# Kernel tuning notes

Measured on AMD Instinct MI355X. Metric: run time of the kernel, lower is better.

## Reference

```python
import jax, jax.numpy as jnp
import numpy as np

B, N, E = 262144, 14, 12
THRESHOLD = 0.3


def setup_inputs() -> dict:
    key = jax.random.key(0)
    k1, k2 = jax.random.split(key)
    pos = jax.random.normal(k1, (B, N, 3), dtype=jnp.float32)
    rot = jax.random.normal(k2, (B, N, 9), dtype=jnp.float32)
    # two 7-node kinematic chains: left arm nodes 0..6, right arm nodes 7..13
    left = np.stack([np.arange(6), np.arange(1, 7)])
    right = np.stack([np.arange(7, 13), np.arange(8, 14)])
    edge_index = jnp.asarray(np.concatenate([left, right], axis=1), dtype=jnp.int32)  # [2, 12]
    ee_mask = jnp.zeros((N, 1), dtype=bool).at[6, 0].set(True).at[13, 0].set(True)
    return {"pos": pos, "rot": rot, "edge_index": edge_index, "ee_mask": ee_mask}


def _capsule_capsule_dist_square(p0, p1, q0, q1):
    # p*: [B, K, 3] left capsules (vary along axis j), q*: [B, K, 3] right capsules (vary along axis i)
    dp = p1 - p0                                  # [B, K, 3]
    dq = q1 - q0                                  # [B, K, 3]
    diff0 = p0[:, None, :, :] - q0[:, :, None, :]  # [B, K(i=q), K(j=p), 3]
    a = jnp.sum(dp * dp, -1)[:, None, :]          # [B, 1, K]
    c = jnp.sum(dq * dq, -1)[:, :, None]          # [B, K, 1]
    b = jnp.einsum('bjd,bid->bij', dp, dq)        # [B, K, K]
    d = jnp.sum(dp[:, None, :, :] * diff0, -1)
    e = jnp.sum(dq[:, :, None, :] * diff0, -1)
    det = a * c - b * b
    bte, ctd, ate, btd = b * e, c * d, a * e, b * d
    s = jnp.zeros_like(det)
    t = jnp.zeros_like(det)
    one = jnp.ones_like(det)
    s = jnp.where((det > 0) & (bte <= ctd) & (e <= 0) & (-d >= a), one, s)
    s = jnp.where((det > 0) & (bte <= ctd) & (e <= 0) & (-d < a) & (-d > 0), -d / a, s)
    t = jnp.where((det > 0) & (bte <= ctd) & (e > 0) & (e < c), e / c, t)
    s = jnp.where((det > 0) & (bte <= ctd) & (e > 0) & (e >= c) & (b - d >= a), one, s)
    s = jnp.where((det > 0) & (bte <= ctd) & (e > 0) & (e >= c) & (b - d < a) & (b - d > 0), (b - d) / a, s)
    t = jnp.where((det > 0) & (bte <= ctd) & (e > 0) & (e >= c), one, t)
    s = jnp.where((det > 0) & (bte > ctd) & (bte - ctd >= det) & (b + e <= 0) & (-d > 0) & (-d < a), -d / a, s)
    s = jnp.where((det > 0) & (bte > ctd) & (bte - ctd >= det) & (b + e <= 0) & (-d > 0) & (-d >= a), one, s)
    s = jnp.where((det > 0) & (bte > ctd) & (bte - ctd >= det) & (b + e > 0) & (b + e < c), one, s)
    t = jnp.where((det > 0) & (bte > ctd) & (bte - ctd >= det) & (b + e > 0) & (b + e < c), (b + e) / c, t)
    s = jnp.where((det > 0) & (bte > ctd) & (bte - ctd >= det) & (b + e > 0) & (b + e >= c) & (b - d > 0) & (b - d < a), (b - d) / a, s)
    s = jnp.where((det > 0) & (bte > ctd) & (bte - ctd >= det) & (b + e > 0) & (b + e >= c) & (b - d > 0) & (b - d >= a), one, s)
    t = jnp.where((det > 0) & (bte > ctd) & (bte - ctd >= det) & (b + e > 0) & (b + e >= c), one, t)
    s = jnp.where((det > 0) & (bte > ctd) & (bte - ctd < det) & (ate <= btd) & (-d > 0) & (-d >= a), one, s)
    s = jnp.where((det > 0) & (bte > ctd) & (bte - ctd < det) & (ate <= btd) & (-d > 0) & (-d < a), -d / a, s)
    s = jnp.where((det > 0) & (bte > ctd) & (bte - ctd < det) & (ate > btd) & (ate - btd >= det) & (b - d > 0) & (b - d >= a), one, s)
    s = jnp.where((det > 0) & (bte > ctd) & (bte - ctd < det) & (ate > btd) & (ate - btd >= det) & (b - d > 0) & (b - d < a), (b - d) / a, s)
    t = jnp.where((det > 0) & (bte > ctd) & (bte - ctd < det) & (ate > btd) & (ate - btd >= det), one, t)
    s = jnp.where((det > 0) & (bte > ctd) & (bte - ctd < det) & (ate > btd) & (ate - btd < det), (bte - ctd) / det, s)
    t = jnp.where((det > 0) & (bte > ctd) & (bte - ctd < det) & (ate > btd) & (ate - btd < det), (ate - btd) / det, t)
    s = jnp.where((det <= 0) & (e <= 0) & (-d > 0) & (-d >= a), one, s)
    s = jnp.where((det <= 0) & (e <= 0) & (-d > 0) & (-d < a), -d / a, s)
    s = jnp.where((det <= 0) & (e > 0) & (e >= c) & (b - d > 0) & (b - d >= a), one, s)
    s = jnp.where((det <= 0) & (e > 0) & (e >= c) & (b - d > 0) & (b - d < a), (b - d) / a, s)
    t = jnp.where((det <= 0) & (e > 0) & (e >= c), one, t)
    t = jnp.where((det <= 0) & (e > 0) & (e < c), e / c, t)
    # original code detaches s and t before forming w
    s = jax.lax.stop_gradient(s)
    t = jax.lax.stop_gradient(t)
    w = diff0 + s[..., None] * dp[:, None, :, :] - t[..., None] * dq[:, :, None, :]
    return jnp.sum(w * w, -1)  # [B, K, K]


def reference(pos, rot, edge_index, ee_mask):
    bsz, n_nodes = pos.shape[0], pos.shape[1]
    n_edges = edge_index.shape[1]
    half = n_edges // 2
    p0 = pos[:, edge_index[0]]  # [B, E, 3]
    p1 = pos[:, edge_index[1]]
    l_p0, r_p0 = p0[:, :half], p0[:, half:]
    l_p1, r_p1 = p1[:, :half], p1[:, half:]
    # exactly 2 end-effectors (left, right) marked in ee_mask
    ee_idx = jnp.nonzero(ee_mask[:, 0], size=2)[0]
    ee_pos = pos[:, ee_idx]                         # [B, 2, 3]  (left, right)
    ee_rot = rot[:, ee_idx].reshape(bsz, 2, 3, 3)   # [B, 2, 3, 3]
    offset = jnp.array([0.0, 0.0, 0.2], dtype=pos.dtype)
    hand_pos = jnp.einsum('beij,j->bei', ee_rot, offset) + ee_pos  # [B, 2, 3]
    l_p0 = jnp.concatenate([l_p0, ee_pos[:, 0:1]], axis=1)   # [B, E/2+1, 3]
    l_p1 = jnp.concatenate([l_p1, hand_pos[:, 0:1]], axis=1)
    r_p0 = jnp.concatenate([r_p0, ee_pos[:, 1:2]], axis=1)
    r_p1 = jnp.concatenate([r_p1, hand_pos[:, 1:2]], axis=1)
    dist_square = _capsule_capsule_dist_square(l_p0, l_p1, r_p0, r_p1)  # [B, 7, 7]
    mask = (dist_square < 0.1 ** 2) & (dist_square > 0)
    special = (dist_square[:, 6, 6] > THRESHOLD ** 2) & (dist_square[:, 6, 6] > 0)
    mask = mask.at[:, 6, 6].set(special)
    loss = jnp.sum(jnp.where(mask, jnp.exp(-dist_square), jnp.zeros_like(dist_square))) / bsz
    return loss
```

## Files before the change

### kernel.cpp

```cpp
#include <hip/hip_runtime.h>


__device__ __forceinline__ float rcpf(float x) { return __builtin_amdgcn_rcpf(x); }
__device__ __forceinline__ float clamp01(float x) {
    return __builtin_amdgcn_fmed3f(x, 0.0f, 1.0f);
}

__device__ __forceinline__ float cap_dist2(
    float px0, float py0, float pz0, float px1, float py1, float pz1,
    float qx0, float qy0, float qz0, float qx1, float qy1, float qz1)
{
    const float dpx = px1 - px0, dpy = py1 - py0, dpz = pz1 - pz0;
    const float dqx = qx1 - qx0, dqy = qy1 - qy0, dqz = qz1 - qz0;
    const float rx  = px0 - qx0, ry  = py0 - qy0, rz  = pz0 - qz0;

    const float a = dpx*dpx + dpy*dpy + dpz*dpz;
    const float c = dqx*dqx + dqy*dqy + dqz*dqz;
    const float b = dpx*dqx + dpy*dqy + dpz*dqz;
    const float d = dpx*rx + dpy*ry + dpz*rz;
    const float e = dqx*rx + dqy*ry + dqz*rz;
    const float det = a*c - b*b;

    const float rcp_a = rcpf(a);
    const float rcp_c = rcpf(c);

    const float f  = b*e - c*d;
    const float s0 = (det > 0.0f) ? clamp01(f * rcpf(det)) : 0.0f;

    const float tn = b*s0 + e;
    const float t  = clamp01(tn * rcp_c);

    const float sA = clamp01(-d * rcp_a);
    const float sB = clamp01((b - d) * rcp_a);
    const float s  = (tn < 0.0f) ? sA : ((tn > c) ? sB : s0);

    const float wx = rx + s*dpx - t*dqx;
    const float wy = ry + s*dpy - t*dqy;
    const float wz = rz + s*dpz - t*dqz;
    return wx*wx + wy*wy + wz*wz;
}

#define BT 128

__global__ __launch_bounds__(BT) void collision_loss_kernel(
    const float* __restrict__ pos,
    const float* __restrict__ rot,
    float* __restrict__ out)
{
    __shared__ float2 sbuf[BT * 21];
    __shared__ float wsum[2];

    const int tid       = threadIdx.x;
    const int blockBase = blockIdx.x * BT;
    const int b         = blockBase + tid;

    const float* rb = rot + (size_t)b * 126;
    const float r6x = rb[ 56], r6y = rb[ 59], r6z = rb[ 62];
    const float rdx = rb[119], rdy = rb[122], rdz = rb[125];

    const float2* g2 = reinterpret_cast<const float2*>(pos + (size_t)blockBase * 42);
    #pragma unroll
    for (int k = 0; k < 21; ++k) {
        const int idx = k * BT + tid;
        sbuf[idx] = g2[idx];
    }
    __syncthreads();

    const float2* m2 = sbuf + tid * 21;
    const float2 u0  = m2[0],  u1  = m2[1],  u2  = m2[2],  u3  = m2[3];
    const float2 u4  = m2[4],  u5  = m2[5],  u6  = m2[6],  u7  = m2[7];
    const float2 u8  = m2[8],  u9  = m2[9],  u10 = m2[10], u11 = m2[11];
    const float2 u12 = m2[12], u13 = m2[13], u14 = m2[14], u15 = m2[15];
    const float2 u16 = m2[16], u17 = m2[17], u18 = m2[18], u19 = m2[19];
    const float2 u20 = m2[20];

    const float n0x=u0.x,  n0y=u0.y,  n0z=u1.x;
    const float n1x=u1.y,  n1y=u2.x,  n1z=u2.y;
    const float n2x=u3.x,  n2y=u3.y,  n2z=u4.x;
    const float n3x=u4.y,  n3y=u5.x,  n3z=u5.y;
    const float n4x=u6.x,  n4y=u6.y,  n4z=u7.x;
    const float n5x=u7.y,  n5y=u8.x,  n5z=u8.y;
    const float n6x=u9.x,  n6y=u9.y,  n6z=u10.x;
    const float n7x=u10.y, n7y=u11.x, n7z=u11.y;
    const float n8x=u12.x, n8y=u12.y, n8z=u13.x;
    const float n9x=u13.y, n9y=u14.x, n9z=u14.y;
    const float n10x=u15.x, n10y=u15.y, n10z=u16.x;
    const float n11x=u16.y, n11y=u17.x, n11z=u17.y;
    const float n12x=u18.x, n12y=u18.y, n12z=u19.x;
    const float n13x=u19.y, n13y=u20.x, n13z=u20.y;

    const float hlx = n6x  + 0.2f * r6x;
    const float hly = n6y  + 0.2f * r6y;
    const float hlz = n6z  + 0.2f * r6z;
    const float hrx = n13x + 0.2f * rdx;
    const float hry = n13y + 0.2f * rdy;
    const float hrz = n13z + 0.2f * rdz;

    float sum = 0.0f;

    auto acc = [&](float p0x, float p0y, float p0z,
                   float p1x, float p1y, float p1z,
                   float q0x, float q0y, float q0z,
                   float q1x, float q1y, float q1z, bool special) {
        const float d2 = cap_dist2(p0x,p0y,p0z, p1x,p1y,p1z,
                                   q0x,q0y,q0z, q1x,q1y,q1z);
        const bool m = special ? (d2 > 0.09f)
                               : ((d2 < 0.01f) && (d2 > 0.0f));
        sum += m ? __expf(-d2) : 0.0f;
    };

    #define LROW(QX0,QY0,QZ0,QX1,QY1,QZ1,SP)                                  \
        acc(n0x,n0y,n0z, n1x,n1y,n1z, QX0,QY0,QZ0, QX1,QY1,QZ1, false);       \
        acc(n1x,n1y,n1z, n2x,n2y,n2z, QX0,QY0,QZ0, QX1,QY1,QZ1, false);       \
        acc(n2x,n2y,n2z, n3x,n3y,n3z, QX0,QY0,QZ0, QX1,QY1,QZ1, false);       \
        acc(n3x,n3y,n3z, n4x,n4y,n4z, QX0,QY0,QZ0, QX1,QY1,QZ1, false);       \
        acc(n4x,n4y,n4z, n5x,n5y,n5z, QX0,QY0,QZ0, QX1,QY1,QZ1, false);       \
        acc(n5x,n5y,n5z, n6x,n6y,n6z, QX0,QY0,QZ0, QX1,QY1,QZ1, false);       \
        acc(n6x,n6y,n6z, hlx,hly,hlz, QX0,QY0,QZ0, QX1,QY1,QZ1, SP);

    LROW(n7x, n7y, n7z,  n8x, n8y, n8z,  false)
    LROW(n8x, n8y, n8z,  n9x, n9y, n9z,  false)
    LROW(n9x, n9y, n9z,  n10x,n10y,n10z, false)
    LROW(n10x,n10y,n10z, n11x,n11y,n11z, false)
    LROW(n11x,n11y,n11z, n12x,n12y,n12z, false)
    LROW(n12x,n12y,n12z, n13x,n13y,n13z, false)
    LROW(n13x,n13y,n13z, hrx, hry, hrz,  true)
    #undef LROW

    #pragma unroll
    for (int off = 32; off > 0; off >>= 1)
        sum += __shfl_down(sum, off, 64);
    const int wave = tid >> 6;
    if ((tid & 63) == 0) wsum[wave] = sum;
    __syncthreads();
    if (tid == 0) {
        atomicAdd(out, (wsum[0] + wsum[1]) * (1.0f / 262144.0f));
    }
}

extern "C" void kernel_launch(void* const* d_in, const int* in_sizes, int n_in,
                              void* d_out, int out_size, void* d_ws, size_t ws_size,
                              hipStream_t stream) {
    const float* pos = (const float*)d_in[0];
    const float* rot = (const float*)d_in[1];
    float* out = (float*)d_out;

    const int B = in_sizes[0] / 42;
    hipMemsetAsync(out, 0, sizeof(float), stream);

    collision_loss_kernel<<<B / BT, BT, 0, stream>>>(pos, rot, out);
}
```

Baseline: 218.4 us.

## Process two batch tiles per block with register prefetch and per-wave LDS slabs

```diff
diff --git a/kernel.cpp b/kernel.cpp
--- a/kernel.cpp
+++ b/kernel.cpp
@@ -41,32 +41,13 @@
 }
 
 #define BT 128
+#define PB 2
 
-__global__ __launch_bounds__(BT) void collision_loss_kernel(
-    const float* __restrict__ pos,
-    const float* __restrict__ rot,
-    float* __restrict__ out)
+__device__ __forceinline__ float phase_compute(
+    const float2* __restrict__ m2,
+    float r6x, float r6y, float r6z,
+    float rdx, float rdy, float rdz)
 {
-    __shared__ float2 sbuf[BT * 21];
-    __shared__ float wsum[2];
-
-    const int tid       = threadIdx.x;
-    const int blockBase = blockIdx.x * BT;
-    const int b         = blockBase + tid;
-
-    const float* rb = rot + (size_t)b * 126;
-    const float r6x = rb[ 56], r6y = rb[ 59], r6z = rb[ 62];
-    const float rdx = rb[119], rdy = rb[122], rdz = rb[125];
-
-    const float2* g2 = reinterpret_cast<const float2*>(pos + (size_t)blockBase * 42);
-    #pragma unroll
-    for (int k = 0; k < 21; ++k) {
-        const int idx = k * BT + tid;
-        sbuf[idx] = g2[idx];
-    }
-    __syncthreads();
-
-    const float2* m2 = sbuf + tid * 21;
     const float2 u0  = m2[0],  u1  = m2[1],  u2  = m2[2],  u3  = m2[3];
     const float2 u4  = m2[4],  u5  = m2[5],  u6  = m2[6],  u7  = m2[7];
     const float2 u8  = m2[8],  u9  = m2[9],  u10 = m2[10], u11 = m2[11];
@@ -96,9 +77,9 @@
     const float hry = n13y + 0.2f * rdy;
     const float hrz = n13z + 0.2f * rdz;
 
-    float sum = 0.0f;
+    float sum0 = 0.0f, sum1 = 0.0f;
 
-    auto acc = [&](float p0x, float p0y, float p0z,
+    auto acc = [&](float& s_, float p0x, float p0y, float p0z,
                    float p1x, float p1y, float p1z,
                    float q0x, float q0y, float q0z,
                    float q1x, float q1y, float q1z, bool special) {
@@ -106,32 +87,82 @@
                                    q0x,q0y,q0z, q1x,q1y,q1z);
         const bool m = special ? (d2 > 0.09f)
                                : ((d2 < 0.01f) && (d2 > 0.0f));
-        sum += m ? __expf(-d2) : 0.0f;
+        s_ += m ? __expf(-d2) : 0.0f;
     };
 
-    #define LROW(QX0,QY0,QZ0,QX1,QY1,QZ1,SP)                                  \
-        acc(n0x,n0y,n0z, n1x,n1y,n1z, QX0,QY0,QZ0, QX1,QY1,QZ1, false);       \
-        acc(n1x,n1y,n1z, n2x,n2y,n2z, QX0,QY0,QZ0, QX1,QY1,QZ1, false);       \
-        acc(n2x,n2y,n2z, n3x,n3y,n3z, QX0,QY0,QZ0, QX1,QY1,QZ1, false);       \
-        acc(n3x,n3y,n3z, n4x,n4y,n4z, QX0,QY0,QZ0, QX1,QY1,QZ1, false);       \
-        acc(n4x,n4y,n4z, n5x,n5y,n5z, QX0,QY0,QZ0, QX1,QY1,QZ1, false);       \
-        acc(n5x,n5y,n5z, n6x,n6y,n6z, QX0,QY0,QZ0, QX1,QY1,QZ1, false);       \
-        acc(n6x,n6y,n6z, hlx,hly,hlz, QX0,QY0,QZ0, QX1,QY1,QZ1, SP);
+    #define LROW(S, QX0,QY0,QZ0,QX1,QY1,QZ1,SP)                                  \
+        acc(S, n0x,n0y,n0z, n1x,n1y,n1z, QX0,QY0,QZ0, QX1,QY1,QZ1, false);       \
+        acc(S, n1x,n1y,n1z, n2x,n2y,n2z, QX0,QY0,QZ0, QX1,QY1,QZ1, false);       \
+        acc(S, n2x,n2y,n2z, n3x,n3y,n3z, QX0,QY0,QZ0, QX1,QY1,QZ1, false);       \
+        acc(S, n3x,n3y,n3z, n4x,n4y,n4z, QX0,QY0,QZ0, QX1,QY1,QZ1, false);       \
+        acc(S, n4x,n4y,n4z, n5x,n5y,n5z, QX0,QY0,QZ0, QX1,QY1,QZ1, false);       \
+        acc(S, n5x,n5y,n5z, n6x,n6y,n6z, QX0,QY0,QZ0, QX1,QY1,QZ1, false);       \
+        acc(S, n6x,n6y,n6z, hlx,hly,hlz, QX0,QY0,QZ0, QX1,QY1,QZ1, SP);
 
-    LROW(n7x, n7y, n7z,  n8x, n8y, n8z,  false)
-    LROW(n8x, n8y, n8z,  n9x, n9y, n9z,  false)
-    LROW(n9x, n9y, n9z,  n10x,n10y,n10z, false)
-    LROW(n10x,n10y,n10z, n11x,n11y,n11z, false)
-    LROW(n11x,n11y,n11z, n12x,n12y,n12z, false)
-    LROW(n12x,n12y,n12z, n13x,n13y,n13z, false)
-    LROW(n13x,n13y,n13z, hrx, hry, hrz,  true)
+    LROW(sum0, n7x, n7y, n7z,  n8x, n8y, n8z,  false)
+    LROW(sum1, n8x, n8y, n8z,  n9x, n9y, n9z,  false)
+    LROW(sum0, n9x, n9y, n9z,  n10x,n10y,n10z, false)
+    LROW(sum1, n10x,n10y,n10z, n11x,n11y,n11z, false)
+    LROW(sum0, n11x,n11y,n11z, n12x,n12y,n12z, false)
+    LROW(sum1, n12x,n12y,n12z, n13x,n13y,n13z, false)
+    LROW(sum0, n13x,n13y,n13z, hrx, hry, hrz,  true)
     #undef LROW
+
+    return sum0 + sum1;
+}
+
+__global__ __launch_bounds__(BT) void collision_loss_kernel(
+    const float* __restrict__ pos,
+    const float* __restrict__ rot,
+    float* __restrict__ out)
+{
+    __shared__ float2 sbuf[2][64 * 21];
+    __shared__ float wsum[2];
+
+    const int tid  = threadIdx.x;
+    const int lane = tid & 63;
+    const int wave = tid >> 6;
+    const int blockBase = blockIdx.x * (BT * PB);
+
+    float2* slab = sbuf[wave];
+
+    const int rowBase0 = blockBase + wave * 64;
+    const int rowBase1 = blockBase + BT + wave * 64;
+
+    const float2* g0  = reinterpret_cast<const float2*>(pos + (size_t)rowBase0 * 42);
+    const float2* g1  = reinterpret_cast<const float2*>(pos + (size_t)rowBase1 * 42);
+    const float*  rb0 = rot + (size_t)(rowBase0 + lane) * 126;
+    const float*  rb1 = rot + (size_t)(rowBase1 + lane) * 126;
+
+    float2 ld0[21];
+    #pragma unroll
+    for (int k = 0; k < 21; ++k) ld0[k] = g0[k * 64 + lane];
+
+    const float a6x = rb0[ 56], a6y = rb0[ 59], a6z = rb0[ 62];
+    const float adx = rb0[119], ady = rb0[122], adz = rb0[125];
+    const float b6x = rb1[ 56], b6y = rb1[ 59], b6z = rb1[ 62];
+    const float bdx = rb1[119], bdy = rb1[122], bdz = rb1[125];
+
+    float2 ld1[21];
+    #pragma unroll
+    for (int k = 0; k < 21; ++k) ld1[k] = g1[k * 64 + lane];
+
+    #pragma unroll
+    for (int k = 0; k < 21; ++k) slab[k * 64 + lane] = ld0[k];
+
+    const float2* m2 = slab + (size_t)lane * 21;
+
+    float sum = phase_compute(m2, a6x, a6y, a6z, adx, ady, adz);
+
+    #pragma unroll
+    for (int k = 0; k < 21; ++k) slab[k * 64 + lane] = ld1[k];
+
+    sum += phase_compute(m2, b6x, b6y, b6z, bdx, bdy, bdz);
 
     #pragma unroll
     for (int off = 32; off > 0; off >>= 1)
         sum += __shfl_down(sum, off, 64);
-    const int wave = tid >> 6;
-    if ((tid & 63) == 0) wsum[wave] = sum;
+    if (lane == 0) wsum[wave] = sum;
     __syncthreads();
     if (tid == 0) {
         atomicAdd(out, (wsum[0] + wsum[1]) * (1.0f / 262144.0f));
@@ -148,5 +179,5 @@
     const int B = in_sizes[0] / 42;
     hipMemsetAsync(out, 0, sizeof(float), stream);
 
-    collision_loss_kernel<<<B / BT, BT, 0, stream>>>(pos, rot, out);
+    collision_loss_kernel<<<B / (BT * PB), BT, 0, stream>>>(pos, rot, out);
 }
```

New measurement: 224.3 us. +2.7%, slower.

## Use per-wave LDS slabs, rolled right-arm loop, and split accumulators

Applied to the files above, without the earlier changes.

```diff
diff --git a/kernel.cpp b/kernel.cpp
--- a/kernel.cpp
+++ b/kernel.cpp
@@ -40,39 +40,41 @@
     return wx*wx + wy*wy + wz*wz;
 }
 
-#define BT 128
+#define BT 256
 
 __global__ __launch_bounds__(BT) void collision_loss_kernel(
     const float* __restrict__ pos,
     const float* __restrict__ rot,
     float* __restrict__ out)
 {
-    __shared__ float2 sbuf[BT * 21];
-    __shared__ float wsum[2];
+    __shared__ float2 sbuf[4][64 * 21];
+    __shared__ float wsum[4];
 
-    const int tid       = threadIdx.x;
+    const int tid  = threadIdx.x;
+    const int lane = tid & 63;
+    const int wave = tid >> 6;
     const int blockBase = blockIdx.x * BT;
-    const int b         = blockBase + tid;
+    const int slabBase  = blockBase + wave * 64;
 
-    const float* rb = rot + (size_t)b * 126;
+    float2* slab = sbuf[wave];
+
+    const float2* g2 = reinterpret_cast<const float2*>(pos + (size_t)slabBase * 42);
+    float2 ld[21];
+    #pragma unroll
+    for (int k = 0; k < 21; ++k) ld[k] = g2[k * 64 + lane];
+
+    const float* rb = rot + (size_t)(slabBase + lane) * 126;
     const float r6x = rb[ 56], r6y = rb[ 59], r6z = rb[ 62];
     const float rdx = rb[119], rdy = rb[122], rdz = rb[125];
 
-    const float2* g2 = reinterpret_cast<const float2*>(pos + (size_t)blockBase * 42);
     #pragma unroll
-    for (int k = 0; k < 21; ++k) {
-        const int idx = k * BT + tid;
-        sbuf[idx] = g2[idx];
-    }
-    __syncthreads();
+    for (int k = 0; k < 21; ++k) slab[k * 64 + lane] = ld[k];
 
-    const float2* m2 = sbuf + tid * 21;
+    const float2* m2 = slab + (size_t)lane * 21;
     const float2 u0  = m2[0],  u1  = m2[1],  u2  = m2[2],  u3  = m2[3];
     const float2 u4  = m2[4],  u5  = m2[5],  u6  = m2[6],  u7  = m2[7];
-    const float2 u8  = m2[8],  u9  = m2[9],  u10 = m2[10], u11 = m2[11];
-    const float2 u12 = m2[12], u13 = m2[13], u14 = m2[14], u15 = m2[15];
-    const float2 u16 = m2[16], u17 = m2[17], u18 = m2[18], u19 = m2[19];
-    const float2 u20 = m2[20];
+    const float2 u8  = m2[8],  u9  = m2[9],  u10 = m2[10];
+    const float2 u19 = m2[19], u20 = m2[20];
 
     const float n0x=u0.x,  n0y=u0.y,  n0z=u1.x;
     const float n1x=u1.y,  n1y=u2.x,  n1z=u2.y;
@@ -81,12 +83,6 @@
     const float n4x=u6.x,  n4y=u6.y,  n4z=u7.x;
     const float n5x=u7.y,  n5y=u8.x,  n5z=u8.y;
     const float n6x=u9.x,  n6y=u9.y,  n6z=u10.x;
-    const float n7x=u10.y, n7y=u11.x, n7z=u11.y;
-    const float n8x=u12.x, n8y=u12.y, n8z=u13.x;
-    const float n9x=u13.y, n9y=u14.x, n9z=u14.y;
-    const float n10x=u15.x, n10y=u15.y, n10z=u16.x;
-    const float n11x=u16.y, n11y=u17.x, n11z=u17.y;
-    const float n12x=u18.x, n12y=u18.y, n12z=u19.x;
     const float n13x=u19.y, n13y=u20.x, n13z=u20.y;
 
     const float hlx = n6x  + 0.2f * r6x;
@@ -96,9 +92,9 @@
     const float hry = n13y + 0.2f * rdy;
     const float hrz = n13z + 0.2f * rdz;
 
-    float sum = 0.0f;
+    float sum0 = 0.0f, sum1 = 0.0f;
 
-    auto acc = [&](float p0x, float p0y, float p0z,
+    auto acc = [&](float& s_, float p0x, float p0y, float p0z,
                    float p1x, float p1y, float p1z,
                    float q0x, float q0y, float q0z,
                    float q1x, float q1y, float q1z, bool special) {
@@ -106,35 +102,40 @@
                                    q0x,q0y,q0z, q1x,q1y,q1z);
         const bool m = special ? (d2 > 0.09f)
                                : ((d2 < 0.01f) && (d2 > 0.0f));
-        sum += m ? __expf(-d2) : 0.0f;
+        s_ += m ? __expf(-d2) : 0.0f;
     };
 
     #define LROW(QX0,QY0,QZ0,QX1,QY1,QZ1,SP)                                  \
-        acc(n0x,n0y,n0z, n1x,n1y,n1z, QX0,QY0,QZ0, QX1,QY1,QZ1, false);       \
-        acc(n1x,n1y,n1z, n2x,n2y,n2z, QX0,QY0,QZ0, QX1,QY1,QZ1, false);       \
-        acc(n2x,n2y,n2z, n3x,n3y,n3z, QX0,QY0,QZ0, QX1,QY1,QZ1, false);       \
-        acc(n3x,n3y,n3z, n4x,n4y,n4z, QX0,QY0,QZ0, QX1,QY1,QZ1, false);       \
-        acc(n4x,n4y,n4z, n5x,n5y,n5z, QX0,QY0,QZ0, QX1,QY1,QZ1, false);       \
-        acc(n5x,n5y,n5z, n6x,n6y,n6z, QX0,QY0,QZ0, QX1,QY1,QZ1, false);       \
-        acc(n6x,n6y,n6z, hlx,hly,hlz, QX0,QY0,QZ0, QX1,QY1,QZ1, SP);
+        acc(sum0, n0x,n0y,n0z, n1x,n1y,n1z, QX0,QY0,QZ0, QX1,QY1,QZ1, false); \
+        acc(sum1, n1x,n1y,n1z, n2x,n2y,n2z, QX0,QY0,QZ0, QX1,QY1,QZ1, false); \
+        acc(sum0, n2x,n2y,n2z, n3x,n3y,n3z, QX0,QY0,QZ0, QX1,QY1,QZ1, false); \
+        acc(sum1, n3x,n3y,n3z, n4x,n4y,n4z, QX0,QY0,QZ0, QX1,QY1,QZ1, false); \
+        acc(sum0, n4x,n4y,n4z, n5x,n5y,n5z, QX0,QY0,QZ0, QX1,QY1,QZ1, false); \
+        acc(sum1, n5x,n5y,n5z, n6x,n6y,n6z, QX0,QY0,QZ0, QX1,QY1,QZ1, false); \
+        acc(sum0, n6x,n6y,n6z, hlx,hly,hlz, QX0,QY0,QZ0, QX1,QY1,QZ1, SP);
 
-    LROW(n7x, n7y, n7z,  n8x, n8y, n8z,  false)
-    LROW(n8x, n8y, n8z,  n9x, n9y, n9z,  false)
-    LROW(n9x, n9y, n9z,  n10x,n10y,n10z, false)
-    LROW(n10x,n10y,n10z, n11x,n11y,n11z, false)
-    LROW(n11x,n11y,n11z, n12x,n12y,n12z, false)
-    LROW(n12x,n12y,n12z, n13x,n13y,n13z, false)
-    LROW(n13x,n13y,n13z, hrx, hry, hrz,  true)
+    const float* sf = reinterpret_cast<const float*>(slab) + (size_t)lane * 42;
+    #pragma clang loop unroll(disable)
+    for (int i = 0; i < 6; ++i) {
+        const int f0 = 21 + 3 * i;
+        const float q0x = sf[f0    ], q0y = sf[f0 + 1], q0z = sf[f0 + 2];
+        const float q1x = sf[f0 + 3], q1y = sf[f0 + 4], q1z = sf[f0 + 5];
+        LROW(q0x,q0y,q0z, q1x,q1y,q1z, false)
+    }
+
+    LROW(n13x,n13y,n13z, hrx,hry,hrz, true)
     #undef LROW
+
+    float sum = sum0 + sum1;
 
     #pragma unroll
     for (int off = 32; off > 0; off >>= 1)
         sum += __shfl_down(sum, off, 64);
-    const int wave = tid >> 6;
-    if ((tid & 63) == 0) wsum[wave] = sum;
+    if (lane == 0) wsum[wave] = sum;
     __syncthreads();
     if (tid == 0) {
-        atomicAdd(out, (wsum[0] + wsum[1]) * (1.0f / 262144.0f));
+        atomicAdd(out, (wsum[0] + wsum[1] + wsum[2] + wsum[3])
+                       * (1.0f / 262144.0f));
     }
 }
 
```

New measurement: 214.7 us, median of 2. Within noise of the previous version (-1.7%).
